# Kernel optimization log

Measured on AMD Instinct MI355X. Metric: run time of the kernel, lower is better.

The kernel has to match this reference:

```python
import jax, jax.numpy as jnp
import numpy as np
import math

B, T, D, DA = 4, 4096, 1024, 64
N_LAYERS = 12  # scaling uses sqrt(DA) * 12 per the original module


def setup_inputs() -> dict:
    key = jax.random.key(0)
    ks = jax.random.split(key, 7)
    s = 1.0 / math.sqrt(D)
    return {
        "x": jax.random.normal(ks[0], (B, T, D), dtype=jnp.float32),
        "Wq": jax.random.normal(ks[1], (D, DA), dtype=jnp.float32) * s,
        "bq": jax.random.normal(ks[2], (DA,), dtype=jnp.float32) * 0.01,
        "Wk": jax.random.normal(ks[3], (D, DA), dtype=jnp.float32) * s,
        "bk": jax.random.normal(ks[4], (DA,), dtype=jnp.float32) * 0.01,
        "Wv": jax.random.normal(ks[5], (D, DA), dtype=jnp.float32) * s,
        "bv": jax.random.normal(ks[6], (DA,), dtype=jnp.float32) * 0.01,
    }


def reference(x, Wq, bq, Wk, bk, Wv, bv):
    # x: [B, T, D]
    q = jnp.einsum('btd,da->bta', x, Wq) + bq  # [B, T, DA]
    k = jnp.einsum('btd,da->bta', x, Wk) + bk
    v = jnp.einsum('btd,da->bta', x, Wv) + bv
    scale = 1.0 / (math.sqrt(DA) * N_LAYERS)
    scores = jnp.einsum('bqa,bka->bqk', q, k) * scale  # [B, T, T]
    causal = jnp.tril(jnp.ones((T, T), dtype=bool))
    scores = jnp.where(causal[None, :, :], scores, -jnp.inf)
    attn = jax.nn.softmax(scores, axis=-1)
    return jnp.einsum('bqk,bka->bqa', attn, v)  # [B, T, DA]
```

## Files before the change

kernel.cpp:

```cpp
#include <hip/hip_runtime.h>
#include <hip/hip_bf16.h>


#define T_SEQ 4096
#define NW 12

using bf16x8 = __bf16 __attribute__((ext_vector_type(8)));
using f32x16 = float __attribute__((ext_vector_type(16)));
using uint4v = unsigned int __attribute__((ext_vector_type(4)));

static constexpr float QSCALE = 1.4426950408889634f / 96.0f;

__device__ __forceinline__ unsigned short bf1(float v) {
    unsigned u = __builtin_bit_cast(unsigned, v);
    u += 0x7FFFu + ((u >> 16) & 1u);
    return (unsigned short)(u >> 16);
}
__device__ __forceinline__ unsigned cvt2(float lo, float hi) {
    unsigned r;
    asm("v_cvt_pk_bf16_f32 %0, %1, %2" : "=v"(r) : "v"(lo), "v"(hi));
    return r;
}
__device__ __forceinline__ void pswap(unsigned& a, unsigned& b) {
    asm volatile("v_permlane32_swap_b32 %0, %1" : "+v"(a), "+v"(b));
}
__device__ __forceinline__ float bflo(unsigned u) {
    return __builtin_bit_cast(float, u << 16);
}
__device__ __forceinline__ float bfhi(unsigned u) {
    return __builtin_bit_cast(float, u & 0xFFFF0000u);
}
__device__ __forceinline__ f32x16 zero16() {
    f32x16 z;
#pragma unroll
    for (int i = 0; i < 16; ++i) z[i] = 0.0f;
    return z;
}
#define MFMA32(a, b, c) __builtin_amdgcn_mfma_f32_32x32x16_bf16(a, b, c, 0, 0, 0)

__device__ __forceinline__ void gload_lds16(const float* g, float* l) {
    __builtin_amdgcn_global_load_lds(
        (const __attribute__((address_space(1))) float*)g,
        (__attribute__((address_space(3))) float*)l, 16, 0, 0);
}

__global__ __launch_bounds__(256) void prep_w(
        const float* __restrict__ Wq, const float* __restrict__ Wk,
        const float* __restrict__ Wv, const float* __restrict__ bq,
        const float* __restrict__ bk, const float* __restrict__ bv,
        unsigned short* __restrict__ Wt3, float* __restrict__ bias_t) {
    __shared__ float tile[64][65];
    const int tid = threadIdx.x;
    const int m = blockIdx.x >> 4, kt = blockIdx.x & 15, d0 = kt * 64;
    const float* W = (m == 0) ? Wq : (m == 1) ? Wk : Wv;
    const int a = tid & 63, r4 = tid >> 6;
#pragma unroll
    for (int j = 0; j < 16; ++j) {
        const int rr = r4 + 4 * j;
        tile[rr][a] = W[(size_t)(d0 + rr) * 64 + a];
    }
    __syncthreads();
    const float scl = (m == 0) ? QSCALE : 1.0f;
    const int dc = tid & 63, ar = tid >> 6;
#pragma unroll
    for (int j = 0; j < 16; ++j) {
        const int aa = ar + 4 * j;
        const int cg = m * 64 + aa;
        const size_t addr =
            ((size_t)(kt * 6 + (cg >> 5)) * 4 + (dc >> 4)) * 512 +
            ((cg & 31) + 32 * ((dc >> 3) & 1)) * 8 + (dc & 7);
        Wt3[addr] = bf1(tile[dc][aa] * scl);
    }
    if (kt == 0 && tid < 64) {
        const float* bb = (m == 0) ? bq : (m == 1) ? bk : bv;
        bias_t[m * 64 + tid] = bb[tid] * scl;
    }
}

__global__ __launch_bounds__(384, 3) void proj_kernel(
        const float* __restrict__ x, const unsigned short* __restrict__ Wt3,
        const float* __restrict__ bias_t, unsigned short* __restrict__ qs,
        unsigned short* __restrict__ ksf, unsigned short* __restrict__ vtf) {
    __shared__ float Ald[3][2048];

    const int tid = threadIdx.x;
    const int w = tid >> 6, l = tid & 63, g = l >> 5, c32 = l & 31;
    const int ct = w;
    const int rowbase = blockIdx.x * 32;

    const int j1 = w;
    const int row1 = 4 * j1 + (l >> 4);
    const float* gp1 = x + (size_t)(rowbase + row1) * 1024 +
                       (((l & 15) ^ (row1 & 7)) << 2);
    const bool has2 = (w < 2);
    const int j2 = 6 + w;
    const int row2 = 4 * j2 + (l >> 4);
    const float* gp2 = x + (size_t)(rowbase + row2) * 1024 +
                       (((l & 15) ^ (row2 & 7)) << 2);

    const unsigned short* Wb = Wt3 + (size_t)(ct * 4) * 512 + l * 8;

    f32x16 acc = zero16();
    bf16x8 bA[4], bB[4];

    gload_lds16(gp1, &Ald[0][j1 * 256]);
    if (has2) gload_lds16(gp2, &Ald[0][j2 * 256]);
    gload_lds16(gp1 + 64, &Ald[1][j1 * 256]);
    if (has2) gload_lds16(gp2 + 64, &Ald[1][j2 * 256]);
#pragma unroll
    for (int f = 0; f < 4; ++f) bA[f] = *(const bf16x8*)(Wb + f * 512);
    if (has2) asm volatile("s_waitcnt vmcnt(6)" ::: "memory");
    else      asm volatile("s_waitcnt vmcnt(5)" ::: "memory");
    __builtin_amdgcn_s_barrier();
    __builtin_amdgcn_sched_barrier(0);

    auto STAGE = [&](bf16x8(&bc)[4], bf16x8(&bn)[4], int kt) {
        if (kt < 15) {
            const unsigned short* Wn = Wb + (size_t)(kt + 1) * 12288;
#pragma unroll
            for (int f = 0; f < 4; ++f) bn[f] = *(const bf16x8*)(Wn + f * 512);
        }
        if (kt < 14) {
            gload_lds16(gp1 + (kt + 2) * 64, &Ald[(kt + 2) % 3][j1 * 256]);
            if (has2)
                gload_lds16(gp2 + (kt + 2) * 64, &Ald[(kt + 2) % 3][j2 * 256]);
        }
        const float* A = Ald[kt % 3];
#pragma unroll
        for (int kk = 0; kk < 4; ++kk) {
            const int blk = kk * 4 + g * 2;
            float4 f0 = *(const float4*)(A + c32 * 64 + ((blk ^ (c32 & 7)) << 2));
            float4 f1 = *(const float4*)(A + c32 * 64 + (((blk + 1) ^ (c32 & 7)) << 2));
            uint4v ua;
            ua[0] = cvt2(f0.x, f0.y); ua[1] = cvt2(f0.z, f0.w);
            ua[2] = cvt2(f1.x, f1.y); ua[3] = cvt2(f1.z, f1.w);
            bf16x8 af = __builtin_bit_cast(bf16x8, ua);
            acc = MFMA32(af, bc[kk], acc);
        }
        if (kt < 14) {
            if (has2) asm volatile("s_waitcnt vmcnt(6) lgkmcnt(0)" ::: "memory");
            else      asm volatile("s_waitcnt vmcnt(5) lgkmcnt(0)" ::: "memory");
            __builtin_amdgcn_s_barrier();
            __builtin_amdgcn_sched_barrier(0);
        } else if (kt == 14) {
            asm volatile("s_waitcnt vmcnt(4) lgkmcnt(0)" ::: "memory");
            __builtin_amdgcn_s_barrier();
            __builtin_amdgcn_sched_barrier(0);
        }
    };

#pragma unroll
    for (int kt = 0; kt < 16; kt += 2) {
        STAGE(bA, bB, kt);
        STAGE(bB, bA, kt + 1);
    }

    const int cg = ct * 32 + c32;
    const float bias = bias_t[cg];
    const int mat = cg >> 6, cm = cg & 63;
    if (mat == 2) {
#pragma unroll
        for (int q4 = 0; q4 < 4; ++q4) {
            const int rowg = rowbase + 8 * q4 + 4 * g;
            const int b = rowg >> 12, tl = rowg & (T_SEQ - 1);
            const int ch = tl >> 5;
            const int f = (cm >> 5) * 2 + (q4 >> 1);
            const int lane = (cm & 31) + 32 * (q4 & 1);
            unsigned lo = cvt2(acc[4 * q4 + 0] + bias, acc[4 * q4 + 1] + bias);
            unsigned hi = cvt2(acc[4 * q4 + 2] + bias, acc[4 * q4 + 3] + bias);
            *(uint2*)(vtf + ((size_t)b * 128 + ch) * 2048 + f * 512 +
                      lane * 8 + 4 * g) = make_uint2(lo, hi);
        }
    } else if (mat == 1) {
#pragma unroll
        for (int r = 0; r < 16; ++r) {
            const int rowg = rowbase + (r & 3) + 8 * (r >> 2) + 4 * g;
            const int b = rowg >> 12, tl = rowg & (T_SEQ - 1);
            ksf[((size_t)b * 128 + (tl >> 5)) * 2048 + (cm >> 4) * 512 +
                ((tl & 31) + 32 * ((cm >> 3) & 1)) * 8 + (cm & 7)] =
                bf1(acc[r] + bias);
        }
    } else {
#pragma unroll
        for (int r = 0; r < 16; ++r) {
            const int rowg = rowbase + (r & 3) + 8 * (r >> 2) + 4 * g;
            qs[(size_t)rowg * 64 + cm] = bf1(acc[r] + bias);
        }
    }
}

__global__ __launch_bounds__(768, 3) void attn_kernel(
        const unsigned short* __restrict__ qs, const unsigned short* __restrict__ ksf,
        const unsigned short* __restrict__ vtf, float* __restrict__ out) {
    __shared__ unsigned short Osh[NW][32][66];
    __shared__ float msh[NW][32];
    __shared__ float ssh[NW][32];

    const int tid = threadIdx.x;
    const int w = tid >> 6, l = tid & 63, g = l >> 5, c32 = l & 31;
    const int b = blockIdx.x & 3;
    const int pid = blockIdx.x >> 2;

    for (int tt = 0; tt < 2; ++tt) {
        const int jt = tt ? pid : 127 - pid;
        const int qbase = jt * 32;

        const unsigned short* qp =
            qs + ((size_t)b * T_SEQ + qbase + c32) * 64 + g * 8;
        bf16x8 qf[4];
#pragma unroll
        for (int t = 0; t < 4; ++t) qf[t] = *(const bf16x8*)(qp + 16 * t);

        const unsigned short* pKc = ksf + ((size_t)b * 128 + w) * 2048 + l * 8;
        const unsigned short* pVc = vtf + ((size_t)b * 128 + w) * 2048 + l * 8;

        auto loadK = [&](bf16x8(&kf)[4]) {
#pragma unroll
            for (int t = 0; t < 4; ++t)
                kf[t] = *(const bf16x8*)(pKc + t * 512);
            pKc += NW * 2048;
        };
        auto loadV = [&](bf16x8(&vf)[4]) {
#pragma unroll
            for (int f = 0; f < 4; ++f)
                vf[f] = *(const bf16x8*)(pVc + f * 512);
            pVc += NW * 2048;
        };

        const int nch = (jt >= w) ? (jt - w) / NW + 1 : 0;
        const bool hasDiag = (jt >= w) && ((jt - w) % NW == 0);
        float m = -INFINITY, ssum = 0.0f;
        f32x16 o0 = zero16(), o1 = zero16();
        f32x16 s_cur;
        bf16x8 k0[4], k1[4], vR[4];

        if (nch > 0) {
            loadK(k0);
            f32x16 t = zero16();
#pragma unroll
            for (int t4 = 0; t4 < 4; ++t4) t = MFMA32(k0[t4], qf[t4], t);
            s_cur = t;
        }

        auto STEP = [&](bf16x8(&kn)[4], int i) {
            loadV(vR);
            if (i + 1 < nch) loadK(kn);
            if (hasDiag && i == nch - 1) {
#pragma unroll
                for (int r = 0; r < 16; ++r) {
                    const int kl = (r & 3) + 8 * (r >> 2) + 4 * g;
                    if (kl > c32) s_cur[r] = -1e30f;
                }
            }
            float a0 = fmaxf(fmaxf(s_cur[0], s_cur[1]), fmaxf(s_cur[2], s_cur[3]));
            float a1 = fmaxf(fmaxf(s_cur[4], s_cur[5]), fmaxf(s_cur[6], s_cur[7]));
            float a2 = fmaxf(fmaxf(s_cur[8], s_cur[9]), fmaxf(s_cur[10], s_cur[11]));
            float a3 = fmaxf(fmaxf(s_cur[12], s_cur[13]), fmaxf(s_cur[14], s_cur[15]));
            float pm = fmaxf(fmaxf(a0, a1), fmaxf(a2, a3));
            if (!__all(pm <= m + 8.0f)) {
                float rmax = fmaxf(pm, __shfl_xor(pm, 32, 64));
                const float mn = fmaxf(m, rmax);
                const float alpha = exp2f(m - mn);
#pragma unroll
                for (int r = 0; r < 16; ++r) { o0[r] *= alpha; o1[r] *= alpha; }
                ssum *= alpha;
                m = mn;
            }
            float p[16];
#pragma unroll
            for (int r = 0; r < 16; ++r) p[r] = exp2f(s_cur[r] - m);
            float s0 = (p[0] + p[1]) + (p[2] + p[3]);
            float s1 = (p[4] + p[5]) + (p[6] + p[7]);
            float s2 = (p[8] + p[9]) + (p[10] + p[11]);
            float s3 = (p[12] + p[13]) + (p[14] + p[15]);
            ssum += (s0 + s1) + (s2 + s3);
            unsigned c01 = cvt2(p[0], p[1]), c23 = cvt2(p[2], p[3]);
            unsigned c45 = cvt2(p[4], p[5]), c67 = cvt2(p[6], p[7]);
            pswap(c01, c45); pswap(c23, c67);
            unsigned c89 = cvt2(p[8], p[9]), cab = cvt2(p[10], p[11]);
            unsigned ccd = cvt2(p[12], p[13]), cef = cvt2(p[14], p[15]);
            pswap(c89, ccd); pswap(cab, cef);
            uint4v u0; u0[0] = c01; u0[1] = c23; u0[2] = c45; u0[3] = c67;
            uint4v u1; u1[0] = c89; u1[1] = cab; u1[2] = ccd; u1[3] = cef;
            bf16x8 pb0 = __builtin_bit_cast(bf16x8, u0);
            bf16x8 pb1 = __builtin_bit_cast(bf16x8, u1);
            __builtin_amdgcn_s_setprio(1);
            o0 = MFMA32(vR[0], pb0, o0);
            o0 = MFMA32(vR[1], pb1, o0);
            o1 = MFMA32(vR[2], pb0, o1);
            o1 = MFMA32(vR[3], pb1, o1);
            if (i + 1 < nch) {
                f32x16 t = zero16();
#pragma unroll
                for (int t4 = 0; t4 < 4; ++t4) t = MFMA32(kn[t4], qf[t4], t);
                s_cur = t;
            }
            __builtin_amdgcn_s_setprio(0);
        };

        int i = 0;
        while (i < nch) {
            STEP(k1, i); ++i;
            if (i < nch) { STEP(k0, i); ++i; }
        }
        ssum += __shfl_xor(ssum, 32, 64);

        if (l < 32) { msh[w][l] = m; ssh[w][l] = ssum; }
#pragma unroll
        for (int q4 = 0; q4 < 4; ++q4) {
            const int base = 8 * q4 + 4 * g;
            *(unsigned*)&Osh[w][c32][base]      = cvt2(o0[4 * q4], o0[4 * q4 + 1]);
            *(unsigned*)&Osh[w][c32][base + 2]  = cvt2(o0[4 * q4 + 2], o0[4 * q4 + 3]);
            *(unsigned*)&Osh[w][c32][base + 32] = cvt2(o1[4 * q4], o1[4 * q4 + 1]);
            *(unsigned*)&Osh[w][c32][base + 34] = cvt2(o1[4 * q4 + 2], o1[4 * q4 + 3]);
        }
        __syncthreads();

        if (tid < 512) {
            const int qrow = tid >> 4, e4 = tid & 15;
            float M = -INFINITY;
            float mw[NW];
#pragma unroll
            for (int u = 0; u < NW; ++u) { mw[u] = msh[u][qrow]; M = fmaxf(M, mw[u]); }
            float den = 0.0f;
            float r0 = 0.f, r1 = 0.f, r2 = 0.f, r3 = 0.f;
#pragma unroll
            for (int u = 0; u < NW; ++u) {
                const float scu = exp2f(mw[u] - M);
                den += ssh[u][qrow] * scu;
                const unsigned ua = *(const unsigned*)&Osh[u][qrow][4 * e4];
                const unsigned ub = *(const unsigned*)&Osh[u][qrow][4 * e4 + 2];
                r0 += bflo(ua) * scu;
                r1 += bfhi(ua) * scu;
                r2 += bflo(ub) * scu;
                r3 += bfhi(ub) * scu;
            }
            const float inv = 1.0f / den;
            float4 st;
            st.x = r0 * inv; st.y = r1 * inv; st.z = r2 * inv; st.w = r3 * inv;
            *(float4*)(out + ((size_t)b * T_SEQ + qbase + qrow) * 64 + 4 * e4) = st;
        }
        __syncthreads();
    }
}

extern "C" void kernel_launch(void* const* d_in, const int* in_sizes, int n_in,
                              void* d_out, int out_size, void* d_ws, size_t ws_size,
                              hipStream_t stream) {
    const float* x  = (const float*)d_in[0];
    const float* Wq = (const float*)d_in[1];
    const float* bq = (const float*)d_in[2];
    const float* Wk = (const float*)d_in[3];
    const float* bk = (const float*)d_in[4];
    const float* Wv = (const float*)d_in[5];
    const float* bv = (const float*)d_in[6];
    float* out = (float*)d_out;

    char* ws = (char*)d_ws;
    unsigned short* Wt3    = (unsigned short*)(ws);
    float*          bias_t = (float*)(ws + 393216);
    unsigned short* qsb    = (unsigned short*)(ws + (1u << 20));
    unsigned short* ksb    = (unsigned short*)(ws + (3u << 20));
    unsigned short* vtb    = (unsigned short*)(ws + (5u << 20));

    prep_w<<<48, 256, 0, stream>>>(Wq, Wk, Wv, bq, bk, bv, Wt3, bias_t);
    proj_kernel<<<512, 384, 0, stream>>>(x, Wt3, bias_t, qsb, ksb, vtb);
    attn_kernel<<<256, 768, 0, stream>>>(qsb, ksb, vtb, out);
}
```

Measured before the change: 49.16 us.

## Use 8 waves per block and process key chunks in pairs per iteration

Cuts the attention block from 12 to 8 waves (512 threads) and replaces the software-pipelined single-chunk loop with a loop that loads two K/V chunks at once. It computes both score tiles, takes one shared max and rescale, then does the PV MFMAs for both, with a tail path for an odd chunk count. The aim is more independent MFMA and memory work per iteration and fewer rescale checks. In exchange it drops the previous prefetch overlap of the next K chunk, raises per-wave register pressure, and each wave now handles more chunks.

```diff
diff --git a/kernel.cpp b/kernel.cpp
--- a/kernel.cpp
+++ b/kernel.cpp
@@ -3,7 +3,7 @@
 
 
 #define T_SEQ 4096
-#define NW 12
+#define NW 8
 
 using bf16x8 = __bf16 __attribute__((ext_vector_type(8)));
 using f32x16 = float __attribute__((ext_vector_type(16)));
@@ -189,7 +189,7 @@
     }
 }
 
-__global__ __launch_bounds__(768, 3) void attn_kernel(
+__global__ __launch_bounds__(512, 2) void attn_kernel(
         const unsigned short* __restrict__ qs, const unsigned short* __restrict__ ksf,
         const unsigned short* __restrict__ vtf, float* __restrict__ out) {
     __shared__ unsigned short Osh[NW][32][66];
@@ -214,49 +214,14 @@
         const unsigned short* pKc = ksf + ((size_t)b * 128 + w) * 2048 + l * 8;
         const unsigned short* pVc = vtf + ((size_t)b * 128 + w) * 2048 + l * 8;
 
-        auto loadK = [&](bf16x8(&kf)[4]) {
-#pragma unroll
-            for (int t = 0; t < 4; ++t)
-                kf[t] = *(const bf16x8*)(pKc + t * 512);
-            pKc += NW * 2048;
-        };
-        auto loadV = [&](bf16x8(&vf)[4]) {
-#pragma unroll
-            for (int f = 0; f < 4; ++f)
-                vf[f] = *(const bf16x8*)(pVc + f * 512);
-            pVc += NW * 2048;
-        };
-
         const int nch = (jt >= w) ? (jt - w) / NW + 1 : 0;
         const bool hasDiag = (jt >= w) && ((jt - w) % NW == 0);
+        const int npair = nch >> 1;
+        const bool tailOdd = (nch & 1) != 0;
         float m = -INFINITY, ssum = 0.0f;
         f32x16 o0 = zero16(), o1 = zero16();
-        f32x16 s_cur;
-        bf16x8 k0[4], k1[4], vR[4];
-
-        if (nch > 0) {
-            loadK(k0);
-            f32x16 t = zero16();
-#pragma unroll
-            for (int t4 = 0; t4 < 4; ++t4) t = MFMA32(k0[t4], qf[t4], t);
-            s_cur = t;
-        }
-
-        auto STEP = [&](bf16x8(&kn)[4], int i) {
-            loadV(vR);
-            if (i + 1 < nch) loadK(kn);
-            if (hasDiag && i == nch - 1) {
-#pragma unroll
-                for (int r = 0; r < 16; ++r) {
-                    const int kl = (r & 3) + 8 * (r >> 2) + 4 * g;
-                    if (kl > c32) s_cur[r] = -1e30f;
-                }
-            }
-            float a0 = fmaxf(fmaxf(s_cur[0], s_cur[1]), fmaxf(s_cur[2], s_cur[3]));
-            float a1 = fmaxf(fmaxf(s_cur[4], s_cur[5]), fmaxf(s_cur[6], s_cur[7]));
-            float a2 = fmaxf(fmaxf(s_cur[8], s_cur[9]), fmaxf(s_cur[10], s_cur[11]));
-            float a3 = fmaxf(fmaxf(s_cur[12], s_cur[13]), fmaxf(s_cur[14], s_cur[15]));
-            float pm = fmaxf(fmaxf(a0, a1), fmaxf(a2, a3));
+
+        auto DEFER = [&](float pm) {
             if (!__all(pm <= m + 8.0f)) {
                 float rmax = fmaxf(pm, __shfl_xor(pm, 32, 64));
                 const float mn = fmaxf(m, rmax);
@@ -266,9 +231,18 @@
                 ssum *= alpha;
                 m = mn;
             }
+        };
+        auto TREEMAX = [&](const f32x16& s) {
+            float a0 = fmaxf(fmaxf(s[0], s[1]), fmaxf(s[2], s[3]));
+            float a1 = fmaxf(fmaxf(s[4], s[5]), fmaxf(s[6], s[7]));
+            float a2 = fmaxf(fmaxf(s[8], s[9]), fmaxf(s[10], s[11]));
+            float a3 = fmaxf(fmaxf(s[12], s[13]), fmaxf(s[14], s[15]));
+            return fmaxf(fmaxf(a0, a1), fmaxf(a2, a3));
+        };
+        auto EXPPACK = [&](const f32x16& s, bf16x8& pb0, bf16x8& pb1) {
             float p[16];
 #pragma unroll
-            for (int r = 0; r < 16; ++r) p[r] = exp2f(s_cur[r] - m);
+            for (int r = 0; r < 16; ++r) p[r] = exp2f(s[r] - m);
             float s0 = (p[0] + p[1]) + (p[2] + p[3]);
             float s1 = (p[4] + p[5]) + (p[6] + p[7]);
             float s2 = (p[8] + p[9]) + (p[10] + p[11]);
@@ -282,26 +256,81 @@
             pswap(c89, ccd); pswap(cab, cef);
             uint4v u0; u0[0] = c01; u0[1] = c23; u0[2] = c45; u0[3] = c67;
             uint4v u1; u1[0] = c89; u1[1] = cab; u1[2] = ccd; u1[3] = cef;
-            bf16x8 pb0 = __builtin_bit_cast(bf16x8, u0);
-            bf16x8 pb1 = __builtin_bit_cast(bf16x8, u1);
+            pb0 = __builtin_bit_cast(bf16x8, u0);
+            pb1 = __builtin_bit_cast(bf16x8, u1);
+        };
+
+        for (int j = 0; j < npair; ++j) {
+            bf16x8 kA[4], kB[4], vA[4], vB[4];
+#pragma unroll
+            for (int t = 0; t < 4; ++t) kA[t] = *(const bf16x8*)(pKc + t * 512);
+#pragma unroll
+            for (int t = 0; t < 4; ++t)
+                kB[t] = *(const bf16x8*)(pKc + NW * 2048 + t * 512);
+#pragma unroll
+            for (int f = 0; f < 4; ++f) vA[f] = *(const bf16x8*)(pVc + f * 512);
+#pragma unroll
+            for (int f = 0; f < 4; ++f)
+                vB[f] = *(const bf16x8*)(pVc + NW * 2048 + f * 512);
+            pKc += 2 * NW * 2048;
+            pVc += 2 * NW * 2048;
+            f32x16 sa = zero16(), sb = zero16();
             __builtin_amdgcn_s_setprio(1);
-            o0 = MFMA32(vR[0], pb0, o0);
-            o0 = MFMA32(vR[1], pb1, o0);
-            o1 = MFMA32(vR[2], pb0, o1);
-            o1 = MFMA32(vR[3], pb1, o1);
-            if (i + 1 < nch) {
-                f32x16 t = zero16();
-#pragma unroll
-                for (int t4 = 0; t4 < 4; ++t4) t = MFMA32(kn[t4], qf[t4], t);
-                s_cur = t;
+#pragma unroll
+            for (int t = 0; t < 4; ++t) {
+                sa = MFMA32(kA[t], qf[t], sa);
+                sb = MFMA32(kB[t], qf[t], sb);
             }
             __builtin_amdgcn_s_setprio(0);
-        };
-
-        int i = 0;
-        while (i < nch) {
-            STEP(k1, i); ++i;
-            if (i < nch) { STEP(k0, i); ++i; }
+            if (hasDiag && !tailOdd && j == npair - 1) {
+#pragma unroll
+                for (int r = 0; r < 16; ++r) {
+                    const int kl = (r & 3) + 8 * (r >> 2) + 4 * g;
+                    if (kl > c32) sb[r] = -1e30f;
+                }
+            }
+            DEFER(fmaxf(TREEMAX(sa), TREEMAX(sb)));
+            bf16x8 pa0, pa1, pb0, pb1;
+            EXPPACK(sa, pa0, pa1);
+            EXPPACK(sb, pb0, pb1);
+            __builtin_amdgcn_s_setprio(1);
+            o0 = MFMA32(vA[0], pa0, o0);
+            o1 = MFMA32(vA[2], pa0, o1);
+            o0 = MFMA32(vA[1], pa1, o0);
+            o1 = MFMA32(vA[3], pa1, o1);
+            o0 = MFMA32(vB[0], pb0, o0);
+            o1 = MFMA32(vB[2], pb0, o1);
+            o0 = MFMA32(vB[1], pb1, o0);
+            o1 = MFMA32(vB[3], pb1, o1);
+            __builtin_amdgcn_s_setprio(0);
+        }
+        if (tailOdd) {
+            bf16x8 kA[4], vA[4];
+#pragma unroll
+            for (int t = 0; t < 4; ++t) kA[t] = *(const bf16x8*)(pKc + t * 512);
+#pragma unroll
+            for (int f = 0; f < 4; ++f) vA[f] = *(const bf16x8*)(pVc + f * 512);
+            f32x16 sa = zero16();
+            __builtin_amdgcn_s_setprio(1);
+#pragma unroll
+            for (int t = 0; t < 4; ++t) sa = MFMA32(kA[t], qf[t], sa);
+            __builtin_amdgcn_s_setprio(0);
+            if (hasDiag) {
+#pragma unroll
+                for (int r = 0; r < 16; ++r) {
+                    const int kl = (r & 3) + 8 * (r >> 2) + 4 * g;
+                    if (kl > c32) sa[r] = -1e30f;
+                }
+            }
+            DEFER(TREEMAX(sa));
+            bf16x8 pa0, pa1;
+            EXPPACK(sa, pa0, pa1);
+            __builtin_amdgcn_s_setprio(1);
+            o0 = MFMA32(vA[0], pa0, o0);
+            o1 = MFMA32(vA[2], pa0, o1);
+            o0 = MFMA32(vA[1], pa1, o0);
+            o1 = MFMA32(vA[3], pa1, o1);
+            __builtin_amdgcn_s_setprio(0);
         }
         ssum += __shfl_xor(ssum, 32, 64);
 
@@ -316,7 +345,7 @@
         }
         __syncthreads();
 
-        if (tid < 512) {
+        {
             const int qrow = tid >> 4, e4 = tid & 15;
             float M = -INFINITY;
             float mw[NW];
@@ -365,5 +394,5 @@
 
     prep_w<<<48, 256, 0, stream>>>(Wq, Wk, Wv, bq, bk, bv, Wt3, bias_t);
     proj_kernel<<<512, 384, 0, stream>>>(x, Wt3, bias_t, qsb, ksb, vtb);
-    attn_kernel<<<256, 768, 0, stream>>>(qsb, ksb, vtb, out);
-}
+    attn_kernel<<<256, 512, 0, stream>>>(qsb, ksb, vtb, out);
+}
```

After: 48.54 us. Within noise of the previous version (-1.3%).
